# Optimization experiments

Measured on AMD Instinct MI355X. Metric: run time of the kernel, lower is better.

Reference implementation:

```python
import jax, jax.numpy as jnp
import numpy as np

HIDDEN_DIM = 512  # global scale divisor used in the original layer


def setup_inputs() -> dict:
    key = jax.random.key(0)
    k1, k2 = jax.random.split(key)
    B, S, H = 32, 8192, 512
    states_h = jax.random.normal(k1, (B, H), dtype=jnp.float32)
    enc_out = jax.random.normal(k2, (B, S, H), dtype=jnp.float32)
    return {"states_h": states_h, "enc_out": enc_out}


def reference(states_h, enc_out):
    # align_score = matmul(enc_out, dec_h^T) / hidden_dim -> [B, S, 1]
    align = jnp.einsum("bsh,bh->bs", enc_out, states_h) / HIDDEN_DIM
    # softmax over the sequence axis (axis=1 in the original [B,S,1] tensor)
    weights = jax.nn.softmax(align, axis=1)[:, :, None]           # [B, S, 1]
    # context = sum_s enc_out * weights -> [B, H], then expand to [B, 1, H]
    context = jnp.einsum("bsh,bs->bh", enc_out, weights[:, :, 0])
    context = context[:, None, :]                                  # [B, 1, H]
    return (context, weights)
```

## Files before the change

kernel.cpp:

```cpp
#include <hip/hip_runtime.h>
#include <hip/hip_bf16.h>
#include <math.h>


#define BB 32
#define SS 8192
#define HH 512
#define NB 64
#define WPB 4
#define NP (NB * WPB)
#define RPW (SS / NP)
#define WCH 8

__global__ __launch_bounds__(256, 6) void attn_pass1(
    const float* __restrict__ states, const float* __restrict__ enc,
    float* __restrict__ align, float* __restrict__ pm,
    float* __restrict__ pl, float* __restrict__ pC)
{
    const int b     = blockIdx.x >> 6;
    const int chunk = blockIdx.x & (NB - 1);
    const int lane  = threadIdx.x & 63;
    const int wv    = threadIdx.x >> 6;
    const int p     = chunk * WPB + wv;

    const float4* st = (const float4*)(states + (size_t)b * HH);
    const float4 sh0 = st[lane];
    const float4 sh1 = st[lane + 64];

    const float4* rp = (const float4*)(enc + ((size_t)b * SS + (size_t)p * RPW) * HH);

    float  m = -1e30f, l = 0.0f;
    float4 c0 = make_float4(0.f, 0.f, 0.f, 0.f);
    float4 c1 = make_float4(0.f, 0.f, 0.f, 0.f);
    float  my_a = 0.0f;

    float4 e0 = rp[lane],        e1 = rp[lane + 64];
    float4 f0 = rp[128 + lane],  f1 = rp[128 + lane + 64];

    #pragma unroll 4
    for (int r = 0; r < RPW; ++r) {
        const int rn = (r + 2 < RPW) ? (r + 2) : (RPW - 1);
        const float4* q = rp + (size_t)rn * 128;
        float4 g0 = q[lane];
        float4 g1 = q[lane + 64];

        float d = e0.x*sh0.x + e0.y*sh0.y + e0.z*sh0.z + e0.w*sh0.w
                + e1.x*sh1.x + e1.y*sh1.y + e1.z*sh1.z + e1.w*sh1.w;
        #pragma unroll
        for (int off = 1; off < 64; off <<= 1)
            d += __shfl_xor(d, off, 64);

        float a = d * (1.0f / 512.0f);
        a = __uint_as_float(__builtin_amdgcn_readfirstlane(__float_as_uint(a)));

        my_a = (r == lane) ? a : my_a;

        if (a > m) {
            float sc = __expf(m - a);
            l = fmaf(l, sc, 1.0f);
            c0.x = fmaf(c0.x, sc, e0.x);
            c0.y = fmaf(c0.y, sc, e0.y);
            c0.z = fmaf(c0.z, sc, e0.z);
            c0.w = fmaf(c0.w, sc, e0.w);
            c1.x = fmaf(c1.x, sc, e1.x);
            c1.y = fmaf(c1.y, sc, e1.y);
            c1.z = fmaf(c1.z, sc, e1.z);
            c1.w = fmaf(c1.w, sc, e1.w);
            m = a;
        } else {
            float pr = __expf(a - m);
            l += pr;
            c0.x = fmaf(pr, e0.x, c0.x);
            c0.y = fmaf(pr, e0.y, c0.y);
            c0.z = fmaf(pr, e0.z, c0.z);
            c0.w = fmaf(pr, e0.w, c0.w);
            c1.x = fmaf(pr, e1.x, c1.x);
            c1.y = fmaf(pr, e1.y, c1.y);
            c1.z = fmaf(pr, e1.z, c1.z);
            c1.w = fmaf(pr, e1.w, c1.w);
        }

        e0 = f0; e1 = f1;
        f0 = g0; f1 = g1;
    }

    if (lane < RPW)
        align[(size_t)b * SS + (size_t)p * RPW + lane] = my_a;
    if (lane == 0) {
        pm[b * NP + p] = m;
        pl[b * NP + p] = l;
    }
    float4* Cp = (float4*)(pC + (size_t)(b * NP + p) * HH);
    Cp[lane]      = c0;
    Cp[lane + 64] = c1;
}

__global__ __launch_bounds__(256) void attn_pass2(
    const float* __restrict__ align, const float* __restrict__ pm,
    const float* __restrict__ pl, const float* __restrict__ pC,
    float* __restrict__ out_ctx, float* __restrict__ out_w)
{
    const int b     = blockIdx.x >> 3;
    const int chunk = blockIdx.x & (WCH - 1);
    const int t     = threadIdx.x;
    const int lane  = t & 63;
    const int wv    = t >> 6;

    __shared__ float  s_w[NP];
    __shared__ float  s_red[8];
    __shared__ float  s_bcast[2];
    __shared__ float4 s_part[256];

    float pmv = pm[b * NP + t];
    float plv = pl[b * NP + t];

    float mx = pmv;
    #pragma unroll
    for (int off = 1; off < 64; off <<= 1)
        mx = fmaxf(mx, __shfl_xor(mx, off, 64));
    if (lane == 0) s_red[wv] = mx;
    __syncthreads();
    if (t == 0)
        s_bcast[0] = fmaxf(fmaxf(s_red[0], s_red[1]), fmaxf(s_red[2], s_red[3]));
    __syncthreads();
    const float M = s_bcast[0];

    float swv = __expf(pmv - M);
    s_w[t] = swv;
    float Lp = swv * plv;
    #pragma unroll
    for (int off = 1; off < 64; off <<= 1)
        Lp += __shfl_xor(Lp, off, 64);
    if (lane == 0) s_red[wv] = Lp;
    __syncthreads();
    if (t == 0)
        s_bcast[1] = 1.0f / (s_red[0] + s_red[1] + s_red[2] + s_red[3]);
    __syncthreads();
    const float invL = s_bcast[1];

    {
        const int slot = t & 15;
        const int pg   = t >> 4;
        const float4* Cb4 = (const float4*)(pC + (size_t)b * NP * HH);
        const int colbase = chunk * 16 + slot;
        float4 acc = make_float4(0.f, 0.f, 0.f, 0.f);
        #pragma unroll 4
        for (int p = pg; p < NP; p += 16) {
            float  w = s_w[p];
            float4 v = Cb4[(size_t)p * 128 + colbase];
            acc.x = fmaf(w, v.x, acc.x);
            acc.y = fmaf(w, v.y, acc.y);
            acc.z = fmaf(w, v.z, acc.z);
            acc.w = fmaf(w, v.w, acc.w);
        }
        s_part[t] = acc;
        __syncthreads();
        if (t < 16) {
            float4 tot = make_float4(0.f, 0.f, 0.f, 0.f);
            #pragma unroll
            for (int g = 0; g < 16; ++g) {
                float4 v = s_part[g * 16 + t];
                tot.x += v.x; tot.y += v.y; tot.z += v.z; tot.w += v.w;
            }
            float4* oc4 = (float4*)(out_ctx + (size_t)b * HH);
            oc4[chunk * 16 + t] = make_float4(tot.x * invL, tot.y * invL,
                                              tot.z * invL, tot.w * invL);
        }
    }

    {
        const float4* al4 = (const float4*)(align + (size_t)b * SS + chunk * 1024);
        float4*       ow4 = (float4*)(out_w + (size_t)b * SS + chunk * 1024);
        float4 v = al4[t];
        ow4[t] = make_float4(__expf(v.x - M) * invL, __expf(v.y - M) * invL,
                             __expf(v.z - M) * invL, __expf(v.w - M) * invL);
    }
}

extern "C" void kernel_launch(void* const* d_in, const int* in_sizes, int n_in,
                              void* d_out, int out_size, void* d_ws, size_t ws_size,
                              hipStream_t stream) {
    const float* states = (const float*)d_in[0];
    const float* enc    = (const float*)d_in[1];

    float* out_ctx = (float*)d_out;
    float* out_w   = (float*)d_out + (size_t)BB * HH;

    float* ws_align = (float*)d_ws;
    float* ws_pm    = ws_align + (size_t)BB * SS;
    float* ws_pl    = ws_pm    + (size_t)BB * NP;
    float* ws_pC    = ws_pl    + (size_t)BB * NP;

    attn_pass1<<<BB * NB, 256, 0, stream>>>(states, enc, ws_align, ws_pm, ws_pl, ws_pC);
    attn_pass2<<<BB * WCH, 256, 0, stream>>>(ws_align, ws_pm, ws_pl, ws_pC, out_ctx, out_w);
}
```

Before: 687.2 us.

## Process four rows per group with batched reductions and double-buffered group loads

Pass 1 now handles encoder rows four at a time. The four dot-product wave reductions are interleaved, the online-softmax update uses one rescale per group instead of a branch per row, and loads are double-buffered with two 4-row register sets. This is meant to cut shuffle latency chains, divergent branches and per-row exp/rescale overhead, and to keep more memory loads in flight. In exchange it uses more registers, so the occupancy hint drops from 6 to 4 blocks per CU.

```diff
diff --git a/kernel.cpp b/kernel.cpp
--- a/kernel.cpp
+++ b/kernel.cpp
@@ -10,9 +10,11 @@
 #define WPB 4
 #define NP (NB * WPB)
 #define RPW (SS / NP)
+#define GP 4
+#define NG (RPW / GP)
 #define WCH 8
 
-__global__ __launch_bounds__(256, 6) void attn_pass1(
+__global__ __launch_bounds__(256, 4) void attn_pass1(
     const float* __restrict__ states, const float* __restrict__ enc,
     float* __restrict__ align, float* __restrict__ pm,
     float* __restrict__ pl, float* __restrict__ pC)
@@ -34,55 +36,74 @@
     float4 c1 = make_float4(0.f, 0.f, 0.f, 0.f);
     float  my_a = 0.0f;
 
-    float4 e0 = rp[lane],        e1 = rp[lane + 64];
-    float4 f0 = rp[128 + lane],  f1 = rp[128 + lane + 64];
-
-    #pragma unroll 4
-    for (int r = 0; r < RPW; ++r) {
-        const int rn = (r + 2 < RPW) ? (r + 2) : (RPW - 1);
-        const float4* q = rp + (size_t)rn * 128;
-        float4 g0 = q[lane];
-        float4 g1 = q[lane + 64];
-
-        float d = e0.x*sh0.x + e0.y*sh0.y + e0.z*sh0.z + e0.w*sh0.w
-                + e1.x*sh1.x + e1.y*sh1.y + e1.z*sh1.z + e1.w*sh1.w;
-        #pragma unroll
-        for (int off = 1; off < 64; off <<= 1)
-            d += __shfl_xor(d, off, 64);
-
-        float a = d * (1.0f / 512.0f);
-        a = __uint_as_float(__builtin_amdgcn_readfirstlane(__float_as_uint(a)));
-
-        my_a = (r == lane) ? a : my_a;
-
-        if (a > m) {
-            float sc = __expf(m - a);
-            l = fmaf(l, sc, 1.0f);
-            c0.x = fmaf(c0.x, sc, e0.x);
-            c0.y = fmaf(c0.y, sc, e0.y);
-            c0.z = fmaf(c0.z, sc, e0.z);
-            c0.w = fmaf(c0.w, sc, e0.w);
-            c1.x = fmaf(c1.x, sc, e1.x);
-            c1.y = fmaf(c1.y, sc, e1.y);
-            c1.z = fmaf(c1.z, sc, e1.z);
-            c1.w = fmaf(c1.w, sc, e1.w);
-            m = a;
-        } else {
-            float pr = __expf(a - m);
-            l += pr;
-            c0.x = fmaf(pr, e0.x, c0.x);
-            c0.y = fmaf(pr, e0.y, c0.y);
-            c0.z = fmaf(pr, e0.z, c0.z);
-            c0.w = fmaf(pr, e0.w, c0.w);
-            c1.x = fmaf(pr, e1.x, c1.x);
-            c1.y = fmaf(pr, e1.y, c1.y);
-            c1.z = fmaf(pr, e1.z, c1.z);
-            c1.w = fmaf(pr, e1.w, c1.w);
-        }
-
-        e0 = f0; e1 = f1;
-        f0 = g0; f1 = g1;
-    }
+    float4 A0,A1,A2,A3,A4,A5,A6,A7;
+    float4 B0,B1,B2,B3,B4,B5,B6,B7;
+
+#define LOADG(P0,P1,P2,P3,P4,P5,P6,P7, g) do {                        \
+        const float4* q = rp + (size_t)(g) * (GP * 128) + lane;       \
+        P0 = q[0];   P1 = q[64];                                      \
+        P2 = q[128]; P3 = q[192];                                     \
+        P4 = q[256]; P5 = q[320];                                     \
+        P6 = q[384]; P7 = q[448];                                     \
+    } while (0)
+
+#define DOT8(u, v) ((u).x*sh0.x + (u).y*sh0.y + (u).z*sh0.z + (u).w*sh0.w \
+                  + (v).x*sh1.x + (v).y*sh1.y + (v).z*sh1.z + (v).w*sh1.w)
+
+#define PROCG(P0,P1,P2,P3,P4,P5,P6,P7, g) do {                        \
+        float d0 = DOT8(P0, P1);                                      \
+        float d1 = DOT8(P2, P3);                                      \
+        float d2 = DOT8(P4, P5);                                      \
+        float d3 = DOT8(P6, P7);                                      \
+        _Pragma("unroll")                                             \
+        for (int off = 1; off < 64; off <<= 1) {                      \
+            d0 += __shfl_xor(d0, off, 64);                            \
+            d1 += __shfl_xor(d1, off, 64);                            \
+            d2 += __shfl_xor(d2, off, 64);                            \
+            d3 += __shfl_xor(d3, off, 64);                            \
+        }                                                             \
+        float a0 = d0 * (1.0f / 512.0f);                              \
+        float a1 = d1 * (1.0f / 512.0f);                              \
+        float a2 = d2 * (1.0f / 512.0f);                              \
+        float a3 = d3 * (1.0f / 512.0f);                              \
+        const int rbase = (g) * GP;                                   \
+        my_a = (lane == rbase + 0) ? a0 : my_a;                       \
+        my_a = (lane == rbase + 1) ? a1 : my_a;                       \
+        my_a = (lane == rbase + 2) ? a2 : my_a;                       \
+        my_a = (lane == rbase + 3) ? a3 : my_a;                       \
+        float mg = fmaxf(fmaxf(a0, a1), fmaxf(a2, a3));               \
+        float mn = fmaxf(m, mg);                                      \
+        float sc = __expf(m - mn);            \
+        float p0 = __expf(a0 - mn);                                   \
+        float p1 = __expf(a1 - mn);                                   \
+        float p2 = __expf(a2 - mn);                                   \
+        float p3 = __expf(a3 - mn);                                   \
+        l = fmaf(l, sc, (p0 + p1) + (p2 + p3));                       \
+        float acc;                                                    \
+        acc = p0*P0.x; acc = fmaf(p1,P2.x,acc); acc = fmaf(p2,P4.x,acc); acc = fmaf(p3,P6.x,acc); c0.x = fmaf(c0.x, sc, acc); \
+        acc = p0*P0.y; acc = fmaf(p1,P2.y,acc); acc = fmaf(p2,P4.y,acc); acc = fmaf(p3,P6.y,acc); c0.y = fmaf(c0.y, sc, acc); \
+        acc = p0*P0.z; acc = fmaf(p1,P2.z,acc); acc = fmaf(p2,P4.z,acc); acc = fmaf(p3,P6.z,acc); c0.z = fmaf(c0.z, sc, acc); \
+        acc = p0*P0.w; acc = fmaf(p1,P2.w,acc); acc = fmaf(p2,P4.w,acc); acc = fmaf(p3,P6.w,acc); c0.w = fmaf(c0.w, sc, acc); \
+        acc = p0*P1.x; acc = fmaf(p1,P3.x,acc); acc = fmaf(p2,P5.x,acc); acc = fmaf(p3,P7.x,acc); c1.x = fmaf(c1.x, sc, acc); \
+        acc = p0*P1.y; acc = fmaf(p1,P3.y,acc); acc = fmaf(p2,P5.y,acc); acc = fmaf(p3,P7.y,acc); c1.y = fmaf(c1.y, sc, acc); \
+        acc = p0*P1.z; acc = fmaf(p1,P3.z,acc); acc = fmaf(p2,P5.z,acc); acc = fmaf(p3,P7.z,acc); c1.z = fmaf(c1.z, sc, acc); \
+        acc = p0*P1.w; acc = fmaf(p1,P3.w,acc); acc = fmaf(p2,P5.w,acc); acc = fmaf(p3,P7.w,acc); c1.w = fmaf(c1.w, sc, acc); \
+        m = mn;                                                       \
+    } while (0)
+
+    LOADG(A0,A1,A2,A3,A4,A5,A6,A7, 0);
+    #pragma unroll
+    for (int g = 0; g < NG; g += 2) {
+        LOADG(B0,B1,B2,B3,B4,B5,B6,B7, g + 1);
+        PROCG(A0,A1,A2,A3,A4,A5,A6,A7, g);
+        if (g + 2 < NG)
+            LOADG(A0,A1,A2,A3,A4,A5,A6,A7, g + 2);
+        PROCG(B0,B1,B2,B3,B4,B5,B6,B7, g + 1);
+    }
+
+#undef LOADG
+#undef DOT8
+#undef PROCG
 
     if (lane < RPW)
         align[(size_t)b * SS + (size_t)p * RPW + lane] = my_a;
```

Result: slower. 910.3 us (+32.5%).
